# Optimization experiments

Hardware: AMD Instinct MI355X
Metric: run time of the kernel (lower is better)

The kernel has to match this reference:

```python
import jax, jax.numpy as jnp
import numpy as np

HIDDEN = 1024
N_HEADS = 16
N_LAYERS = 10
LOCAL_K = 3
TOKEN_T, TOKEN_H, TOKEN_W = 4, 16, 16
PATCH_SIZE = 2
LATENT_C = 16
TOKEN_DIM = LATENT_C * PATCH_SIZE * PATCH_SIZE  # 64
TOKEN_IN = TOKEN_DIM + 1                        # 65
N_TOKENS = TOKEN_T * TOKEN_H * TOKEN_W          # 1024
B = 1
HEAD_DIM = HIDDEN // N_HEADS
LN_EPS = 1e-5


def layer_norm(x, w, b):
    m = x.mean(-1, keepdims=True)
    v = ((x - m) ** 2).mean(-1, keepdims=True)
    return (x - m) * jax.lax.rsqrt(v + LN_EPS) * w + b


def patchify(lat):
    Bx, T, C, H, W = lat.shape
    ph, pw = H // PATCH_SIZE, W // PATCH_SIZE
    x = lat.reshape(Bx, T, C, ph, PATCH_SIZE, pw, PATCH_SIZE)
    x = x.transpose(0, 1, 3, 5, 2, 4, 6)
    return x.reshape(Bx, T * ph * pw, C * PATCH_SIZE * PATCH_SIZE)


def unpatchify(tok):
    Bx = tok.shape[0]
    C = TOKEN_DIM // (PATCH_SIZE * PATCH_SIZE)
    x = tok.reshape(Bx, TOKEN_T, TOKEN_H, TOKEN_W, C, PATCH_SIZE, PATCH_SIZE)
    x = x.transpose(0, 1, 4, 2, 5, 3, 6)
    return x.reshape(Bx, TOKEN_T, C, TOKEN_H * PATCH_SIZE, TOKEN_W * PATCH_SIZE)


def gather_neighbors(kv):
    # kv: (B, N, 2D) -> (B, N, 27, 2D), 3x3x3 zero-padded neighborhoods
    Bx, Nx, D2 = kv.shape
    pad = LOCAL_K // 2
    x = kv.reshape(Bx, TOKEN_T, TOKEN_H, TOKEN_W, D2)
    x = jnp.pad(x, ((0, 0), (pad, pad), (pad, pad), (pad, pad), (0, 0)))
    sl = [x[:, dt:dt + TOKEN_T, dh:dh + TOKEN_H, dw:dw + TOKEN_W]
          for dt in range(LOCAL_K) for dh in range(LOCAL_K) for dw in range(LOCAL_K)]
    nb = jnp.stack(sl, axis=4)  # (B,T,H,W,27,2D)
    return nb.reshape(Bx, Nx, LOCAL_K ** 3, D2)


def local_attention(x, qkv_w, out_w):
    Bx, Nx, D = x.shape
    H, d = N_HEADS, HEAD_DIM
    qkv = x @ qkv_w                       # (B,N,3D)
    q, k, v = jnp.split(qkv, 3, axis=-1)
    kv_nb = gather_neighbors(jnp.concatenate([k, v], axis=-1))  # (B,N,27,2D)
    k_nb, v_nb = jnp.split(kv_nb, 2, axis=-1)
    q = q.reshape(Bx, Nx, H, d)
    k_nb = k_nb.reshape(Bx, Nx, LOCAL_K ** 3, H, d)
    v_nb = v_nb.reshape(Bx, Nx, LOCAL_K ** 3, H, d)
    scores = jnp.einsum('bnhd,bnkhd->bnhk', q, k_nb) / np.sqrt(d).astype(np.float32)
    probs = jax.nn.softmax(scores, axis=-1)
    out = jnp.einsum('bnhk,bnkhd->bnhd', probs, v_nb).reshape(Bx, Nx, D)
    return out @ out_w


def global_attention(x, mask_flat, qkv_w, out_w):
    # Each masked query attends to all N keys; math identical to the
    # gather/SDPA/scatter in the original (per-query attention is independent),
    # realized as full attention masked to zero at unmasked positions.
    Bx, Nx, D = x.shape
    H, d = N_HEADS, HEAD_DIM
    qkv = x @ qkv_w
    q, k, v = jnp.split(qkv, 3, axis=-1)
    q = q.reshape(Bx, Nx, H, d)
    k = k.reshape(Bx, Nx, H, d)
    v = v.reshape(Bx, Nx, H, d)
    scores = jnp.einsum('bqhd,bkhd->bhqk', q, k) / np.sqrt(d).astype(np.float32)
    probs = jax.nn.softmax(scores, axis=-1)
    out = jnp.einsum('bhqk,bkhd->bqhd', probs, v).reshape(Bx, Nx, D)
    out = out @ out_w
    return out * mask_flat[..., None].astype(out.dtype)


def setup_inputs() -> dict:
    key = jax.random.key(0)
    ks = jax.random.split(key, 24)
    s = 0.02
    L, D = N_LAYERS, HIDDEN
    inp = {
        'latents': jax.random.normal(ks[0], (B, TOKEN_T, LATENT_C, TOKEN_H * PATCH_SIZE, TOKEN_W * PATCH_SIZE), jnp.float32),
        'token_mask': jax.random.uniform(ks[1], (B, TOKEN_T, TOKEN_H, TOKEN_W)) < 0.1,
        'input_proj_w': jax.random.normal(ks[2], (TOKEN_IN, D), jnp.float32) * s,
        'input_proj_b': jnp.zeros((D,), jnp.float32),
        'emb_t': jax.random.normal(ks[3], (TOKEN_T, D), jnp.float32) * s,
        'emb_h': jax.random.normal(ks[4], (TOKEN_H, D), jnp.float32) * s,
        'emb_w': jax.random.normal(ks[5], (TOKEN_W, D), jnp.float32) * s,
        'ln_local_w': jnp.ones((L, D), jnp.float32),
        'ln_local_b': jnp.zeros((L, D), jnp.float32),
        'ln_global_w': jnp.ones((L, D), jnp.float32),
        'ln_global_b': jnp.zeros((L, D), jnp.float32),
        'ln_ffn_w': jnp.ones((L, D), jnp.float32),
        'ln_ffn_b': jnp.zeros((L, D), jnp.float32),
        'local_qkv_w': jax.random.normal(ks[6], (L, D, 3 * D), jnp.float32) * s,
        'local_out_w': jax.random.normal(ks[7], (L, D, D), jnp.float32) * s,
        'global_qkv_w': jax.random.normal(ks[8], (L, D, 3 * D), jnp.float32) * s,
        'global_out_w': jax.random.normal(ks[9], (L, D, D), jnp.float32) * s,
        'ffn_w1': jax.random.normal(ks[10], (L, D, 4 * D), jnp.float32) * s,
        'ffn_b1': jnp.zeros((L, 4 * D), jnp.float32),
        'ffn_w2': jax.random.normal(ks[11], (L, 4 * D, D), jnp.float32) * s,
        'ffn_b2': jnp.zeros((L, D), jnp.float32),
        'final_ln_w': jnp.ones((D,), jnp.float32),
        'final_ln_b': jnp.zeros((D,), jnp.float32),
        # original zero-inits output_proj; use small random so the test is non-trivial
        'out_proj_w': jax.random.normal(ks[12], (D, TOKEN_DIM), jnp.float32) * s,
        'out_proj_b': jnp.zeros((TOKEN_DIM,), jnp.float32),
    }
    return inp


def reference(latents, token_mask, input_proj_w, input_proj_b, emb_t, emb_h, emb_w,
              ln_local_w, ln_local_b, ln_global_w, ln_global_b, ln_ffn_w, ln_ffn_b,
              local_qkv_w, local_out_w, global_qkv_w, global_out_w,
              ffn_w1, ffn_b1, ffn_w2, ffn_b2, final_ln_w, final_ln_b,
              out_proj_w, out_proj_b):
    Bx = latents.shape[0]
    mask_flat = token_mask.reshape(Bx, -1)
    tokens = patchify(latents)                       # (B, N, TOKEN_DIM)
    flag = mask_flat[..., None].astype(tokens.dtype)
    x = jnp.concatenate([tokens, flag], axis=-1) @ input_proj_w + input_proj_b

    tt, hh, ww = jnp.meshgrid(jnp.arange(TOKEN_T), jnp.arange(TOKEN_H), jnp.arange(TOKEN_W), indexing='ij')
    pos = emb_t[tt.reshape(-1)] + emb_h[hh.reshape(-1)] + emb_w[ww.reshape(-1)]
    x = x + pos[None]

    for l in range(N_LAYERS):
        x = x + local_attention(layer_norm(x, ln_local_w[l], ln_local_b[l]), local_qkv_w[l], local_out_w[l])
        x = x + global_attention(layer_norm(x, ln_global_w[l], ln_global_b[l]), mask_flat, global_qkv_w[l], global_out_w[l])
        h = layer_norm(x, ln_ffn_w[l], ln_ffn_b[l])
        h = jax.nn.gelu(h @ ffn_w1[l] + ffn_b1[l], approximate=False) @ ffn_w2[l] + ffn_b2[l]
        x = x + h

    delta = layer_norm(x, final_ln_w, final_ln_b) @ out_proj_w + out_proj_b
    return unpatchify(tokens + delta)
```

## Files before the change

kernel.cpp:

```cpp
#include <hip/hip_runtime.h>
#include <hip/hip_bf16.h>
#include <math.h>

typedef __bf16 bf16;
typedef __bf16 bf16x8 __attribute__((ext_vector_type(8)));
typedef __bf16 bf16x4 __attribute__((ext_vector_type(4)));
typedef float  f32x4 __attribute__((ext_vector_type(4)));
typedef unsigned int u32x4 __attribute__((ext_vector_type(4)));

#define NTOK 1024
#define HID  1024
#define NH   16
#define HD   64
#define NL   10
#define QCMAX 256

#define EPI_F32  0
#define EPI_GELU 1

__global__ __launch_bounds__(256)
void wtrans_k(const float* __restrict__ W, bf16* __restrict__ Wt, int K, int N)
{
    __shared__ bf16 tile[64][72];
    const long mofs = (long)blockIdx.z * K * N;
    const float* Ws = W + mofs;
    bf16* Wo = Wt + mofs;
    const int n0 = blockIdx.x * 64, k0 = blockIdx.y * 64;
    const int t = threadIdx.x;
    {
        const int r = t >> 2, cc = (t & 3) * 16;
        const float* src = Ws + (long)(k0 + r) * N + n0 + cc;
#pragma unroll
        for (int i = 0; i < 2; ++i) {
            f32x4 a = *(const f32x4*)(src + i * 8);
            f32x4 b = *(const f32x4*)(src + i * 8 + 4);
            bf16x8 w;
            w[0]=(bf16)a.x; w[1]=(bf16)a.y; w[2]=(bf16)a.z; w[3]=(bf16)a.w;
            w[4]=(bf16)b.x; w[5]=(bf16)b.y; w[6]=(bf16)b.z; w[7]=(bf16)b.w;
            *(bf16x8*)&tile[r][cc + i * 8] = w;
        }
    }
    __syncthreads();
    {
        const int n = t >> 2, kc = (t & 3) * 16;
        bf16x8 o0, o1;
#pragma unroll
        for (int j = 0; j < 8; ++j) { o0[j] = tile[kc + j][n]; o1[j] = tile[kc + 8 + j][n]; }
        bf16* dst = Wo + (long)(n0 + n) * K + k0 + kc;
        *(bf16x8*)dst = o0;
        *(bf16x8*)(dst + 8) = o1;
    }
}

template<int EPI, int BM, int BN, int KSPLIT>
__global__ __launch_bounds__(256)
void gemm_k(const bf16* __restrict__ A, int lda, long bsA,
            const bf16* __restrict__ Bt, int ldb, long bsB,
            void* __restrict__ Cv, int ldc, long bsC,
            const float* __restrict__ bias, int K)
{
    constexpr int WC  = (BM == 128) ? 2 : 4;
    constexpr int WTN = BN / WC;
    constexpr int NF  = WTN / 16;
    __shared__ bf16 Al[2][BM * 32];
    __shared__ bf16 Bl[2][BN * 32];

    const int t    = threadIdx.x;
    const int lane = t & 63;
    const int wv   = t >> 6;
    const int wr   = wv / WC, wc = wv % WC;
    const int lrow = lane & 15, lk = lane >> 4;
    const int n0   = blockIdx.x * BN;
    const int m0   = blockIdx.y * BM;
    const int ks   = (KSPLIT > 1) ? (blockIdx.z % KSPLIT) : 0;
    const int bz   = (KSPLIT > 1) ? (blockIdx.z / KSPLIT) : blockIdx.z;
    const int Kc   = K / KSPLIT;

    const bf16* Ab = A  + bsA * bz + (long)ks * Kc;
    const bf16* Bb = Bt + bsB * bz + (long)ks * Kc;

    f32x4 acc[4][NF];
#pragma unroll
    for (int m = 0; m < 4; ++m)
#pragma unroll
        for (int n = 0; n < NF; ++n) acc[m][n] = f32x4{0.f, 0.f, 0.f, 0.f};

    const int sr = t >> 2, sc = (t & 3) * 8;

    auto stage = [&](int buf, int kk) {
#pragma unroll
        for (int i = 0; i < BM / 64; ++i)
            __builtin_amdgcn_global_load_lds(
                (const __attribute__((address_space(1))) void*)(Ab + (long)(m0 + sr + i * 64) * lda + kk + sc),
                (__attribute__((address_space(3))) void*)(&Al[buf][i * 2048 + t * 8]), 16, 0, 0);
#pragma unroll
        for (int i = 0; i < BN / 64; ++i)
            __builtin_amdgcn_global_load_lds(
                (const __attribute__((address_space(1))) void*)(Bb + (long)(n0 + sr + i * 64) * ldb + kk + sc),
                (__attribute__((address_space(3))) void*)(&Bl[buf][i * 2048 + t * 8]), 16, 0, 0);
    };

    stage(0, 0);
    __syncthreads();
    int cur = 0;
    for (int k0 = 0; k0 < Kc; k0 += 32) {
        if (k0 + 32 < Kc) stage(cur ^ 1, k0 + 32);
        bf16x8 af[4], bfv[NF];
#pragma unroll
        for (int m = 0; m < 4; ++m)
            af[m] = *(const bf16x8*)&Al[cur][(wr * 64 + m * 16 + lrow) * 32 + lk * 8];
#pragma unroll
        for (int n = 0; n < NF; ++n)
            bfv[n] = *(const bf16x8*)&Bl[cur][(wc * WTN + n * 16 + lrow) * 32 + lk * 8];
#pragma unroll
        for (int m = 0; m < 4; ++m)
#pragma unroll
            for (int n = 0; n < NF; ++n)
                acc[m][n] = __builtin_amdgcn_mfma_f32_16x16x32_bf16(af[m], bfv[n], acc[m][n], 0, 0, 0);
        __syncthreads();
        cur ^= 1;
    }

    float* Cf = (float*)Cv + bsC * blockIdx.z;
    bf16*  Cb = (bf16*)Cv + bsC * blockIdx.z;
#pragma unroll
    for (int m = 0; m < 4; ++m)
#pragma unroll
        for (int n = 0; n < NF; ++n) {
            const int c = n0 + wc * WTN + n * 16 + lrow;
#pragma unroll
            for (int q = 0; q < 4; ++q) {
                const int r = m0 + wr * 64 + m * 16 + lk * 4 + q;
                const float v = acc[m][n][q];
                const long off = (long)r * ldc + c;
                if (EPI == EPI_F32) Cf[off] = v;
                else {
                    float u = v + bias[c];
                    Cb[off] = (bf16)(0.5f * u * (1.f + erff(u * 0.70710678118654752f)));
                }
            }
        }
}

template<int NS, bool BIAS, bool SCATTER>
__global__ __launch_bounds__(256)
void ln_add_k(float* __restrict__ x, const float* __restrict__ parts, long pstride,
              const float* __restrict__ bias, const int* __restrict__ rmap,
              const float* __restrict__ w, const float* __restrict__ b,
              bf16* __restrict__ o)
{
    int row  = blockIdx.x * 4 + (threadIdx.x >> 6);
    int lane = threadIdx.x & 63;
    f32x4* xr = (f32x4*)(x + (long)row * HID) + lane * 4;
    f32x4 v[4];
#pragma unroll
    for (int i = 0; i < 4; ++i) v[i] = xr[i];

    if (NS > 0) {
        int prow = SCATTER ? rmap[row] : row;
        if (!SCATTER || prow >= 0) {
            const float* pp = parts + (long)prow * 1024 + lane * 16;
#pragma unroll
            for (int ksi = 0; ksi < NS; ++ksi) {
                const f32x4* q = (const f32x4*)(pp + (long)ksi * pstride);
#pragma unroll
                for (int i = 0; i < 4; ++i) v[i] += q[i];
            }
            if (BIAS) {
                const f32x4* bb = (const f32x4*)bias + lane * 4;
#pragma unroll
                for (int i = 0; i < 4; ++i) v[i] += bb[i];
            }
#pragma unroll
            for (int i = 0; i < 4; ++i) xr[i] = v[i];
        }
    }

    float s = 0.f;
#pragma unroll
    for (int i = 0; i < 4; ++i) s += v[i].x + v[i].y + v[i].z + v[i].w;
    for (int m = 32; m; m >>= 1) s += __shfl_xor(s, m);
    float mean = s * (1.f / 1024.f);
    f32x4 d[4];
    float ss = 0.f;
#pragma unroll
    for (int i = 0; i < 4; ++i) {
        d[i] = v[i] - mean;
        ss += d[i].x * d[i].x + d[i].y * d[i].y + d[i].z * d[i].z + d[i].w * d[i].w;
    }
    for (int m = 32; m; m >>= 1) ss += __shfl_xor(ss, m);
    float rs = rsqrtf(ss * (1.f / 1024.f) + 1e-5f);
    const f32x4* wp = (const f32x4*)w + lane * 4;
    const f32x4* bp = (const f32x4*)b + lane * 4;
    bf16x8 o0, o1;
#pragma unroll
    for (int i = 0; i < 4; ++i) {
        f32x4 wv = wp[i], bv = bp[i];
        f32x4 e;
        e.x = d[i].x * rs * wv.x + bv.x; e.y = d[i].y * rs * wv.y + bv.y;
        e.z = d[i].z * rs * wv.z + bv.z; e.w = d[i].w * rs * wv.w + bv.w;
        if (i < 2) { o0[i*4+0]=(bf16)e.x; o0[i*4+1]=(bf16)e.y; o0[i*4+2]=(bf16)e.z; o0[i*4+3]=(bf16)e.w; }
        else       { int k=(i-2)*4; o1[k+0]=(bf16)e.x; o1[k+1]=(bf16)e.y; o1[k+2]=(bf16)e.z; o1[k+3]=(bf16)e.w; }
    }
    bf16* op = o + (long)row * HID + lane * 16;
    *(bf16x8*)op = o0;
    *(bf16x8*)(op + 8) = o1;
}

__global__ __launch_bounds__(256)
void red4pv_k(const float* __restrict__ p, bf16* __restrict__ Oc)
{
    int i = blockIdx.x * 256 + threadIdx.x;
    int d4 = (i & 15) * 4;
    int r  = (i >> 4) & 255;
    int h  = i >> 12;
    const float* base = p + (long)(h * 4) * 16384 + r * 64 + d4;
    f32x4 s = *(const f32x4*)base;
    s += *(const f32x4*)(base + 16384);
    s += *(const f32x4*)(base + 32768);
    s += *(const f32x4*)(base + 49152);
    bf16x4 o;
    o[0] = (bf16)s.x; o[1] = (bf16)s.y; o[2] = (bf16)s.z; o[3] = (bf16)s.w;
    *(bf16x4*)(Oc + (long)r * 1024 + h * 64 + d4) = o;
}

__global__ __launch_bounds__(256)
void lattn_k(const float* __restrict__ qkv, bf16* __restrict__ ao)
{
    int w    = blockIdx.x * 4 + (threadIdx.x >> 6);
    int lane = threadIdx.x & 63;
    int n = w >> 4, h = w & 15;
    int tt = n >> 8, hh = (n >> 4) & 15, ww = n & 15;

    int nj = -1;
    float dotv = 0.f;
    if (lane < 27) {
        int dt = lane / 9 - 1, dh = (lane % 9) / 3 - 1, dw = lane % 3 - 1;
        int t2 = tt + dt, h2 = hh + dh, w2 = ww + dw;
        if (t2 >= 0 && t2 < 4 && h2 >= 0 && h2 < 16 && w2 >= 0 && w2 < 16)
            nj = (t2 << 8) | (h2 << 4) | w2;
    }
    if (nj >= 0) {
        const f32x4* qp = (const f32x4*)(qkv + (long)n * 3072 + h * 64);
        const f32x4* kp = (const f32x4*)(qkv + (long)nj * 3072 + 1024 + h * 64);
#pragma unroll
        for (int i = 0; i < 16; ++i) {
            f32x4 q4 = qp[i], k4 = kp[i];
            dotv += q4.x * k4.x + q4.y * k4.y + q4.z * k4.z + q4.w * k4.w;
        }
    }
    float sc = (lane < 27) ? dotv * 0.125f : -3.0e38f;
    float mx = sc;
    for (int m = 32; m; m >>= 1) mx = fmaxf(mx, __shfl_xor(mx, m));
    float e = (lane < 27) ? __expf(sc - mx) : 0.f;
    float s = e;
    for (int m = 32; m; m >>= 1) s += __shfl_xor(s, m);
    float p = e / s;

    float acc = 0.f;
    for (int j = 0; j < 27; ++j) {
        float pj = __shfl(p, j);
        int  njj = __shfl(nj, j);
        if (njj >= 0) acc += pj * qkv[(long)njj * 3072 + 2048 + h * 64 + lane];
    }
    ao[(long)n * 1024 + h * 64 + lane] = (bf16)acc;
}

__global__ void compact_k(const int* __restrict__ mask, int* __restrict__ qidx,
                          int* __restrict__ rmap)
{
    int lane = threadIdx.x;
    int total = 0;
    for (int base = 0; base < 1024; base += 64) {
        int m = (mask[base + lane] != 0) ? 1 : 0;
        unsigned long long bal = __ballot(m);
        int pos = total + (int)__popcll(bal & ((1ull << lane) - 1ull));
        int ok = (m && pos < QCMAX);
        if (ok) qidx[pos] = base + lane;
        rmap[base + lane] = ok ? pos : -1;
        total += (int)__popcll(bal);
    }
    for (int i = total + lane; i < QCMAX; i += 64) qidx[i] = -1;
}

__global__ __launch_bounds__(256)
void qkvbuild_k(const float* __restrict__ qkv, const int* __restrict__ qidx,
                bf16* __restrict__ Qc, bf16* __restrict__ Kh, bf16* __restrict__ Vt)
{
    __shared__ bf16 vt[64][72];
    const int h = blockIdx.y;
    const int t = threadIdx.x;
    if (blockIdx.x < 4) {
        const int r = blockIdx.x * 64 + (t >> 2), dc = (t & 3) * 16;
        const int q = qidx[r];
        bf16x8 o0, o1;
        if (q >= 0) {
            const f32x4* src = (const f32x4*)(qkv + (long)q * 3072 + h * 64 + dc);
#pragma unroll
            for (int i = 0; i < 2; ++i) {
                f32x4 a = src[i * 2] * 0.125f, b = src[i * 2 + 1] * 0.125f;
                bf16x8 w;
                w[0]=(bf16)a.x; w[1]=(bf16)a.y; w[2]=(bf16)a.z; w[3]=(bf16)a.w;
                w[4]=(bf16)b.x; w[5]=(bf16)b.y; w[6]=(bf16)b.z; w[7]=(bf16)b.w;
                if (i == 0) o0 = w; else o1 = w;
            }
        } else {
#pragma unroll
            for (int j = 0; j < 8; ++j) { o0[j] = (bf16)0.f; o1[j] = (bf16)0.f; }
        }
        bf16* dst = Qc + (long)h * (QCMAX * 64) + (long)r * 64 + dc;
        *(bf16x8*)dst = o0;
        *(bf16x8*)(dst + 8) = o1;
        return;
    }
    const int k0 = (blockIdx.x - 4) * 64;
    {
        const int r = t >> 2, dc = (t & 3) * 16;
        const float* kp = qkv + (long)(k0 + r) * 3072 + 1024 + h * 64 + dc;
        const float* vp = kp + 1024;
        bf16x8 ko0, ko1;
#pragma unroll
        for (int i = 0; i < 2; ++i) {
            f32x4 a = *(const f32x4*)(kp + i * 8);
            f32x4 b = *(const f32x4*)(kp + i * 8 + 4);
            bf16x8 w;
            w[0]=(bf16)a.x; w[1]=(bf16)a.y; w[2]=(bf16)a.z; w[3]=(bf16)a.w;
            w[4]=(bf16)b.x; w[5]=(bf16)b.y; w[6]=(bf16)b.z; w[7]=(bf16)b.w;
            if (i == 0) ko0 = w; else ko1 = w;
        }
        bf16* kd = Kh + (long)h * (NTOK * 64) + (long)(k0 + r) * 64 + dc;
        *(bf16x8*)kd = ko0;
        *(bf16x8*)(kd + 8) = ko1;
#pragma unroll
        for (int i = 0; i < 2; ++i) {
            f32x4 a = *(const f32x4*)(vp + i * 8);
            f32x4 b = *(const f32x4*)(vp + i * 8 + 4);
            bf16x8 w;
            w[0]=(bf16)a.x; w[1]=(bf16)a.y; w[2]=(bf16)a.z; w[3]=(bf16)a.w;
            w[4]=(bf16)b.x; w[5]=(bf16)b.y; w[6]=(bf16)b.z; w[7]=(bf16)b.w;
            *(bf16x8*)&vt[r][dc + i * 8] = w;
        }
    }
    __syncthreads();
    {
        const int d = t >> 2, kc = (t & 3) * 16;
        bf16x8 o0, o1;
#pragma unroll
        for (int j = 0; j < 8; ++j) { o0[j] = vt[kc + j][d]; o1[j] = vt[kc + 8 + j][d]; }
        bf16* dst = Vt + (long)h * (64 * NTOK) + (long)d * NTOK + k0 + kc;
        *(bf16x8*)dst = o0;
        *(bf16x8*)(dst + 8) = o1;
    }
}

__global__ __launch_bounds__(256)
void softmax_k(const float* __restrict__ S, bf16* __restrict__ P)
{
    int row  = blockIdx.x * 4 + (threadIdx.x >> 6);
    int lane = threadIdx.x & 63;
    const f32x4* sp = (const f32x4*)(S + (long)row * 1024) + lane * 4;
    f32x4 v[4];
#pragma unroll
    for (int i = 0; i < 4; ++i) v[i] = sp[i];
    float mx = -3.0e38f;
#pragma unroll
    for (int i = 0; i < 4; ++i)
        mx = fmaxf(mx, fmaxf(fmaxf(v[i].x, v[i].y), fmaxf(v[i].z, v[i].w)));
    for (int m = 32; m; m >>= 1) mx = fmaxf(mx, __shfl_xor(mx, m));
    f32x4 ev[4];
    float sum = 0.f;
#pragma unroll
    for (int i = 0; i < 4; ++i) {
        ev[i].x = __expf(v[i].x - mx); ev[i].y = __expf(v[i].y - mx);
        ev[i].z = __expf(v[i].z - mx); ev[i].w = __expf(v[i].w - mx);
        sum += ev[i].x + ev[i].y + ev[i].z + ev[i].w;
    }
    for (int m = 32; m; m >>= 1) sum += __shfl_xor(sum, m);
    float inv = 1.f / sum;
    bf16x8 o0, o1;
#pragma unroll
    for (int i = 0; i < 4; ++i) {
        f32x4 e = ev[i] * inv;
        if (i < 2) { o0[i*4+0]=(bf16)e.x; o0[i*4+1]=(bf16)e.y; o0[i*4+2]=(bf16)e.z; o0[i*4+3]=(bf16)e.w; }
        else       { int k=(i-2)*4; o1[k+0]=(bf16)e.x; o1[k+1]=(bf16)e.y; o1[k+2]=(bf16)e.z; o1[k+3]=(bf16)e.w; }
    }
    bf16* op = P + (long)row * 1024 + lane * 16;
    *(bf16x8*)op = o0;
    *(bf16x8*)(op + 8) = o1;
}

__global__ __launch_bounds__(256)
void prep_k(const float* __restrict__ lat, const int* __restrict__ mask,
            const float* __restrict__ Wi, const float* __restrict__ bi,
            const float* __restrict__ et, const float* __restrict__ eh,
            const float* __restrict__ ew,
            float* __restrict__ x, float* __restrict__ tokens)
{
    __shared__ float tl[16][65];
    int t = threadIdx.x;
    int n0 = blockIdx.x * 16;
    for (int idx = t; idx < 16 * 65; idx += 256) {
        int ti = idx / 65, d = idx % 65;
        int n = n0 + ti;
        int tt = n >> 8, hh = (n >> 4) & 15, wwi = n & 15;
        float v;
        if (d < 64) {
            int c = d >> 2, ph = (d >> 1) & 1, pw = d & 1;
            v = lat[(((long)tt * 16 + c) * 32 + hh * 2 + ph) * 32 + wwi * 2 + pw];
            tokens[(long)n * 64 + d] = v;
        } else {
            v = mask[n] ? 1.f : 0.f;
        }
        tl[ti][d] = v;
    }
    __syncthreads();
    f32x4 acc[16];
#pragma unroll
    for (int i = 0; i < 16; ++i) acc[i] = f32x4{0.f, 0.f, 0.f, 0.f};
    for (int d = 0; d < 65; ++d) {
        f32x4 wv = *(const f32x4*)(Wi + (long)d * 1024 + t * 4);
#pragma unroll
        for (int ti = 0; ti < 16; ++ti) acc[ti] += tl[ti][d] * wv;
    }
    f32x4 bb = *(const f32x4*)(bi + t * 4);
    for (int ti = 0; ti < 16; ++ti) {
        int n = n0 + ti;
        int tt = n >> 8, hh = (n >> 4) & 15, wwi = n & 15;
        f32x4 pos = *(const f32x4*)(et + (long)tt * 1024 + t * 4)
                  + *(const f32x4*)(eh + (long)hh * 1024 + t * 4)
                  + *(const f32x4*)(ew + (long)wwi * 1024 + t * 4);
        *(f32x4*)(x + (long)n * 1024 + t * 4) = acc[ti] + bb + pos;
    }
}

__global__ __launch_bounds__(256)
void final_k(const bf16* __restrict__ xn, const float* __restrict__ OW,
             const float* __restrict__ ob, const float* __restrict__ tokens,
             float* __restrict__ out)
{
    __shared__ bf16 xl[8][1024];
    __shared__ float part[4][8][64];
    int t = threadIdx.x;
    int n0 = blockIdx.x * 8;
    for (int i = t; i < 1024; i += 256)
        ((u32x4*)xl)[i] = ((const u32x4*)(xn + (long)n0 * 1024))[i];
    __syncthreads();
    int j = t & 63, s = t >> 6;
    float acc[8] = {0.f, 0.f, 0.f, 0.f, 0.f, 0.f, 0.f, 0.f};
    for (int k = s * 256; k < s * 256 + 256; ++k) {
        float w = OW[(long)k * 64 + j];
#pragma unroll
        for (int ti = 0; ti < 8; ++ti) acc[ti] += (float)xl[ti][k] * w;
    }
    for (int ti = 0; ti < 8; ++ti) part[s][ti][j] = acc[ti];
    __syncthreads();
    if (s == 0) {
        for (int ti = 0; ti < 8; ++ti) {
            int n = n0 + ti;
            float v = part[0][ti][j] + part[1][ti][j] + part[2][ti][j] + part[3][ti][j]
                    + ob[j] + tokens[(long)n * 64 + j];
            int tt = n >> 8, hh = (n >> 4) & 15, wwi = n & 15;
            int c = j >> 2, ph = (j >> 1) & 1, pw = j & 1;
            out[(((long)tt * 16 + c) * 32 + hh * 2 + ph) * 32 + wwi * 2 + pw] = v;
        }
    }
}

extern "C" void kernel_launch(void* const* d_in, const int* in_sizes, int n_in,
                              void* d_out, int out_size, void* d_ws, size_t ws_size,
                              hipStream_t stream)
{
    const float* latents = (const float*)d_in[0];
    const int*   mask    = (const int*)d_in[1];
    const float* ipw  = (const float*)d_in[2];
    const float* ipb  = (const float*)d_in[3];
    const float* et   = (const float*)d_in[4];
    const float* eh   = (const float*)d_in[5];
    const float* ew   = (const float*)d_in[6];
    const float* lnlw = (const float*)d_in[7];
    const float* lnlb = (const float*)d_in[8];
    const float* lngw = (const float*)d_in[9];
    const float* lngb = (const float*)d_in[10];
    const float* lnfw = (const float*)d_in[11];
    const float* lnfb = (const float*)d_in[12];
    const float* lqkv = (const float*)d_in[13];
    const float* lout = (const float*)d_in[14];
    const float* gqkv = (const float*)d_in[15];
    const float* gout = (const float*)d_in[16];
    const float* w1   = (const float*)d_in[17];
    const float* b1   = (const float*)d_in[18];
    const float* w2   = (const float*)d_in[19];
    const float* b2   = (const float*)d_in[20];
    const float* flw  = (const float*)d_in[21];
    const float* flb  = (const float*)d_in[22];
    const float* opw  = (const float*)d_in[23];
    const float* opb  = (const float*)d_in[24];

    char* p = (char*)d_ws;
    auto alloc = [&](size_t bytes) { char* r = p; p += (bytes + 255) & ~(size_t)255; return r; };
    float* x      = (float*)alloc((size_t)4 << 20);
    bf16*  xn     = (bf16*)alloc((size_t)2 << 20);
    float* qkv    = (float*)alloc((size_t)12 << 20);
    bf16*  ao     = (bf16*)alloc((size_t)2 << 20);
    bf16*  hbuf   = (bf16*)alloc((size_t)8 << 20);
    float* tokens = (float*)alloc((size_t)256 << 10);
    bf16*  Qc     = (bf16*)alloc((size_t)512 << 10);
    bf16*  Kh     = (bf16*)alloc((size_t)2 << 20);
    bf16*  Vt     = (bf16*)alloc((size_t)2 << 20);
    float* S      = (float*)alloc((size_t)16 << 20);
    bf16*  P      = (bf16*)alloc((size_t)8 << 20);
    bf16*  Oc     = (bf16*)alloc((size_t)512 << 10);
    int*   qidx   = (int*)alloc(4096);
    int*   rmap   = (int*)alloc(4096);
    float* loutp = (float*)alloc((size_t)2 * 1024 * 1024 * 4);
    float* goutp = (float*)alloc((size_t)8 * 256 * 1024 * 4);
    float* pvp   = (float*)alloc((size_t)64 * 256 * 64 * 4);
    float* f2p   = (float*)alloc((size_t)4 * 1024 * 1024 * 4);
    bf16* lqkvT = (bf16*)alloc((size_t)10 * 3072 * 1024 * 2);
    bf16* loutT = (bf16*)alloc((size_t)10 * 1024 * 1024 * 2);
    bf16* gqkvT = (bf16*)alloc((size_t)10 * 3072 * 1024 * 2);
    bf16* goutT = (bf16*)alloc((size_t)10 * 1024 * 1024 * 2);
    bf16* w1T   = (bf16*)alloc((size_t)10 * 4096 * 1024 * 2);
    bf16* w2T   = (bf16*)alloc((size_t)10 * 1024 * 4096 * 2);

    wtrans_k<<<dim3(48, 16, NL), 256, 0, stream>>>(lqkv, lqkvT, 1024, 3072);
    wtrans_k<<<dim3(16, 16, NL), 256, 0, stream>>>(lout, loutT, 1024, 1024);
    wtrans_k<<<dim3(48, 16, NL), 256, 0, stream>>>(gqkv, gqkvT, 1024, 3072);
    wtrans_k<<<dim3(16, 16, NL), 256, 0, stream>>>(gout, goutT, 1024, 1024);
    wtrans_k<<<dim3(64, 16, NL), 256, 0, stream>>>(w1, w1T, 1024, 4096);
    wtrans_k<<<dim3(16, 64, NL), 256, 0, stream>>>(w2, w2T, 4096, 1024);

    prep_k<<<64, 256, 0, stream>>>(latents, mask, ipw, ipb, et, eh, ew, x, tokens);
    compact_k<<<1, 64, 0, stream>>>(mask, qidx, rmap);

    for (int l = 0; l < NL; ++l) {
        const long wq  = (long)l * 3072 * 1024;
        const long wo  = (long)l * 1024 * 1024;
        const long wf1 = (long)l * 4096 * 1024;

        if (l == 0)
            ln_add_k<0, false, false><<<256, 256, 0, stream>>>(
                x, nullptr, 0, nullptr, nullptr, lnlw, lnlb, xn);
        else
            ln_add_k<4, true, false><<<256, 256, 0, stream>>>(
                x, f2p, (long)1024 * 1024, b2 + (l - 1) * 1024, nullptr,
                lnlw + l * HID, lnlb + l * HID, xn);

        gemm_k<EPI_F32, 64, 128, 1><<<dim3(24, 16, 1), 256, 0, stream>>>(
            xn, 1024, 0, lqkvT + wq, 1024, 0, qkv, 3072, 0, nullptr, 1024);
        lattn_k<<<4096, 256, 0, stream>>>(qkv, ao);
        gemm_k<EPI_F32, 64, 128, 2><<<dim3(8, 16, 2), 256, 0, stream>>>(
            ao, 1024, 0, loutT + wo, 1024, 0, loutp, 1024, (long)1024 * 1024, nullptr, 1024);

        ln_add_k<2, false, false><<<256, 256, 0, stream>>>(
            x, loutp, (long)1024 * 1024, nullptr, nullptr,
            lngw + l * HID, lngb + l * HID, xn);

        gemm_k<EPI_F32, 64, 128, 1><<<dim3(24, 16, 1), 256, 0, stream>>>(
            xn, 1024, 0, gqkvT + wq, 1024, 0, qkv, 3072, 0, nullptr, 1024);
        qkvbuild_k<<<dim3(20, 16), 256, 0, stream>>>(qkv, qidx, Qc, Kh, Vt);
        gemm_k<EPI_F32, 64, 128, 1><<<dim3(8, 4, 16), 256, 0, stream>>>(
            Qc, 64, (long)256 * 64, Kh, 64, (long)1024 * 64,
            S, 1024, (long)256 * 1024, nullptr, 64);
        softmax_k<<<1024, 256, 0, stream>>>(S, P);
        gemm_k<EPI_F32, 64, 64, 4><<<dim3(1, 4, 64), 256, 0, stream>>>(
            P, 1024, (long)256 * 1024, Vt, 1024, (long)64 * 1024,
            pvp, 64, (long)256 * 64, nullptr, 1024);
        red4pv_k<<<256, 256, 0, stream>>>(pvp, Oc);
        gemm_k<EPI_F32, 64, 128, 8><<<dim3(8, 4, 8), 256, 0, stream>>>(
            Oc, 1024, 0, goutT + wo, 1024, 0, goutp, 1024, (long)256 * 1024, nullptr, 1024);

        ln_add_k<8, false, true><<<256, 256, 0, stream>>>(
            x, goutp, (long)256 * 1024, nullptr, rmap,
            lnfw + l * HID, lnfb + l * HID, xn);

        gemm_k<EPI_GELU, 64, 128, 1><<<dim3(32, 16, 1), 256, 0, stream>>>(
            xn, 1024, 0, w1T + wf1, 1024, 0, hbuf, 4096, 0, b1 + l * 4096, 1024);
        gemm_k<EPI_F32, 64, 128, 4><<<dim3(8, 16, 4), 256, 0, stream>>>(
            hbuf, 4096, 0, w2T + wf1, 4096, 0, f2p, 1024, (long)1024 * 1024, nullptr, 4096);
    }

    ln_add_k<4, true, false><<<256, 256, 0, stream>>>(
        x, f2p, (long)1024 * 1024, b2 + 9 * 1024, nullptr, flw, flb, xn);
    final_k<<<128, 256, 0, stream>>>(xn, opw, opb, tokens, (float*)d_out);
}
```

Baseline: 2.225 ms.

## Store QKV in bf16, fuse local out-proj residual, merge weight transposes

Both QKV GEMMs now write bf16 output instead of fp32, which halves QKV traffic for the local attention and qkvbuild kernels. The local output projection drops its split-K and adds straight into x through a residual epilogue, removing the partial buffer and the reduction in the next layernorm. The six weight-transpose launches become one kernel with an XOR-swizzled shared tile to cut bank conflicts. In exchange, q and k are rounded to bf16 before the local attention dot products, and the out-proj GEMM launches fewer blocks.

```diff
diff --git a/kernel.cpp b/kernel.cpp
--- a/kernel.cpp
+++ b/kernel.cpp
@@ -10,42 +10,65 @@
 
 #define NTOK 1024
 #define HID  1024
-#define NH   16
-#define HD   64
 #define NL   10
 #define QCMAX 256
 
-#define EPI_F32  0
-#define EPI_GELU 1
-
-__global__ __launch_bounds__(256)
-void wtrans_k(const float* __restrict__ W, bf16* __restrict__ Wt, int K, int N)
-{
-    __shared__ bf16 tile[64][72];
+#define EPI_F32   0
+#define EPI_GELU  1
+#define EPI_RESID 2
+#define EPI_BF16  3
+
+__global__ __launch_bounds__(256)
+void wtransall_k(const float* __restrict__ lqkv, const float* __restrict__ lout,
+                 const float* __restrict__ gqkv, const float* __restrict__ gout,
+                 const float* __restrict__ w1,   const float* __restrict__ w2,
+                 bf16* __restrict__ lqkvT, bf16* __restrict__ loutT,
+                 bf16* __restrict__ gqkvT, bf16* __restrict__ goutT,
+                 bf16* __restrict__ w1T,   bf16* __restrict__ w2T)
+{
+    __shared__ bf16 tile[64 * 64];
+    const int b = blockIdx.x;
+    const float* W; bf16* O; int K, N, ti;
+    if      (b < 768)  { W = lqkv; O = lqkvT; K = 1024; N = 3072; ti = b; }
+    else if (b < 1024) { W = lout; O = loutT; K = 1024; N = 1024; ti = b - 768; }
+    else if (b < 1792) { W = gqkv; O = gqkvT; K = 1024; N = 3072; ti = b - 1024; }
+    else if (b < 2048) { W = gout; O = goutT; K = 1024; N = 1024; ti = b - 1792; }
+    else if (b < 3072) { W = w1;   O = w1T;   K = 1024; N = 4096; ti = b - 2048; }
+    else               { W = w2;   O = w2T;   K = 4096; N = 1024; ti = b - 3072; }
+    const int ntx = N >> 6;
+    const int n0 = (ti % ntx) * 64, k0 = (ti / ntx) * 64;
     const long mofs = (long)blockIdx.z * K * N;
     const float* Ws = W + mofs;
-    bf16* Wo = Wt + mofs;
-    const int n0 = blockIdx.x * 64, k0 = blockIdx.y * 64;
+    bf16* Wo = O + mofs;
     const int t = threadIdx.x;
     {
         const int r = t >> 2, cc = (t & 3) * 16;
+        const int x = (r >> 3) & 7;
+        const int g0 = cc >> 3;
         const float* src = Ws + (long)(k0 + r) * N + n0 + cc;
-#pragma unroll
-        for (int i = 0; i < 2; ++i) {
-            f32x4 a = *(const f32x4*)(src + i * 8);
-            f32x4 b = *(const f32x4*)(src + i * 8 + 4);
-            bf16x8 w;
-            w[0]=(bf16)a.x; w[1]=(bf16)a.y; w[2]=(bf16)a.z; w[3]=(bf16)a.w;
-            w[4]=(bf16)b.x; w[5]=(bf16)b.y; w[6]=(bf16)b.z; w[7]=(bf16)b.w;
-            *(bf16x8*)&tile[r][cc + i * 8] = w;
-        }
+        f32x4 a0 = *(const f32x4*)(src);
+        f32x4 a1 = *(const f32x4*)(src + 4);
+        f32x4 a2 = *(const f32x4*)(src + 8);
+        f32x4 a3 = *(const f32x4*)(src + 12);
+        bf16x8 w0, w1v;
+        w0[0]=(bf16)a0.x; w0[1]=(bf16)a0.y; w0[2]=(bf16)a0.z; w0[3]=(bf16)a0.w;
+        w0[4]=(bf16)a1.x; w0[5]=(bf16)a1.y; w0[6]=(bf16)a1.z; w0[7]=(bf16)a1.w;
+        w1v[0]=(bf16)a2.x; w1v[1]=(bf16)a2.y; w1v[2]=(bf16)a2.z; w1v[3]=(bf16)a2.w;
+        w1v[4]=(bf16)a3.x; w1v[5]=(bf16)a3.y; w1v[6]=(bf16)a3.z; w1v[7]=(bf16)a3.w;
+        *(bf16x8*)&tile[r * 64 + ((g0    ) ^ x) * 8] = w0;
+        *(bf16x8*)&tile[r * 64 + ((g0 | 1) ^ x) * 8] = w1v;
     }
     __syncthreads();
     {
         const int n = t >> 2, kc = (t & 3) * 16;
+        const int g = n >> 3, no = n & 7;
         bf16x8 o0, o1;
 #pragma unroll
-        for (int j = 0; j < 8; ++j) { o0[j] = tile[kc + j][n]; o1[j] = tile[kc + 8 + j][n]; }
+        for (int j = 0; j < 8; ++j) {
+            int r0 = kc + j, r1 = kc + 8 + j;
+            o0[j] = tile[r0 * 64 + ((g ^ ((r0 >> 3) & 7)) * 8) + no];
+            o1[j] = tile[r1 * 64 + ((g ^ ((r1 >> 3) & 7)) * 8) + no];
+        }
         bf16* dst = Wo + (long)(n0 + n) * K + k0 + kc;
         *(bf16x8*)dst = o0;
         *(bf16x8*)(dst + 8) = o1;
@@ -133,7 +156,9 @@
                 const int r = m0 + wr * 64 + m * 16 + lk * 4 + q;
                 const float v = acc[m][n][q];
                 const long off = (long)r * ldc + c;
-                if (EPI == EPI_F32) Cf[off] = v;
+                if (EPI == EPI_F32)        Cf[off] = v;
+                else if (EPI == EPI_BF16)  Cb[off] = (bf16)v;
+                else if (EPI == EPI_RESID) Cf[off] += v;
                 else {
                     float u = v + bias[c];
                     Cb[off] = (bf16)(0.5f * u * (1.f + erff(u * 0.70710678118654752f)));
@@ -225,7 +250,7 @@
 }
 
 __global__ __launch_bounds__(256)
-void lattn_k(const float* __restrict__ qkv, bf16* __restrict__ ao)
+void lattn_k(const bf16* __restrict__ qkv, bf16* __restrict__ ao)
 {
     int w    = blockIdx.x * 4 + (threadIdx.x >> 6);
     int lane = threadIdx.x & 63;
@@ -241,12 +266,13 @@
             nj = (t2 << 8) | (h2 << 4) | w2;
     }
     if (nj >= 0) {
-        const f32x4* qp = (const f32x4*)(qkv + (long)n * 3072 + h * 64);
-        const f32x4* kp = (const f32x4*)(qkv + (long)nj * 3072 + 1024 + h * 64);
-#pragma unroll
-        for (int i = 0; i < 16; ++i) {
-            f32x4 q4 = qp[i], k4 = kp[i];
-            dotv += q4.x * k4.x + q4.y * k4.y + q4.z * k4.z + q4.w * k4.w;
+        const bf16x8* qp = (const bf16x8*)(qkv + (long)n * 3072 + h * 64);
+        const bf16x8* kp = (const bf16x8*)(qkv + (long)nj * 3072 + 1024 + h * 64);
+#pragma unroll
+        for (int i = 0; i < 8; ++i) {
+            bf16x8 q8 = qp[i], k8 = kp[i];
+#pragma unroll
+            for (int j = 0; j < 8; ++j) dotv += (float)q8[j] * (float)k8[j];
         }
     }
     float sc = (lane < 27) ? dotv * 0.125f : -3.0e38f;
@@ -261,7 +287,7 @@
     for (int j = 0; j < 27; ++j) {
         float pj = __shfl(p, j);
         int  njj = __shfl(nj, j);
-        if (njj >= 0) acc += pj * qkv[(long)njj * 3072 + 2048 + h * 64 + lane];
+        if (njj >= 0) acc += pj * (float)qkv[(long)njj * 3072 + 2048 + h * 64 + lane];
     }
     ao[(long)n * 1024 + h * 64 + lane] = (bf16)acc;
 }
@@ -284,7 +310,7 @@
 }
 
 __global__ __launch_bounds__(256)
-void qkvbuild_k(const float* __restrict__ qkv, const int* __restrict__ qidx,
+void qkvbuild_k(const bf16* __restrict__ qkv, const int* __restrict__ qidx,
                 bf16* __restrict__ Qc, bf16* __restrict__ Kh, bf16* __restrict__ Vt)
 {
     __shared__ bf16 vt[64][72];
@@ -295,14 +321,12 @@
         const int q = qidx[r];
         bf16x8 o0, o1;
         if (q >= 0) {
-            const f32x4* src = (const f32x4*)(qkv + (long)q * 3072 + h * 64 + dc);
-#pragma unroll
-            for (int i = 0; i < 2; ++i) {
-                f32x4 a = src[i * 2] * 0.125f, b = src[i * 2 + 1] * 0.125f;
-                bf16x8 w;
-                w[0]=(bf16)a.x; w[1]=(bf16)a.y; w[2]=(bf16)a.z; w[3]=(bf16)a.w;
-                w[4]=(bf16)b.x; w[5]=(bf16)b.y; w[6]=(bf16)b.z; w[7]=(bf16)b.w;
-                if (i == 0) o0 = w; else o1 = w;
+            const bf16x8* src = (const bf16x8*)(qkv + (long)q * 3072 + h * 64 + dc);
+            bf16x8 a = src[0], b = src[1];
+#pragma unroll
+            for (int j = 0; j < 8; ++j) {
+                o0[j] = (bf16)((float)a[j] * 0.125f);
+                o1[j] = (bf16)((float)b[j] * 0.125f);
             }
         } else {
 #pragma unroll
@@ -316,30 +340,14 @@
     const int k0 = (blockIdx.x - 4) * 64;
     {
         const int r = t >> 2, dc = (t & 3) * 16;
-        const float* kp = qkv + (long)(k0 + r) * 3072 + 1024 + h * 64 + dc;
-        const float* vp = kp + 1024;
-        bf16x8 ko0, ko1;
-#pragma unroll
-        for (int i = 0; i < 2; ++i) {
-            f32x4 a = *(const f32x4*)(kp + i * 8);
-            f32x4 b = *(const f32x4*)(kp + i * 8 + 4);
-            bf16x8 w;
-            w[0]=(bf16)a.x; w[1]=(bf16)a.y; w[2]=(bf16)a.z; w[3]=(bf16)a.w;
-            w[4]=(bf16)b.x; w[5]=(bf16)b.y; w[6]=(bf16)b.z; w[7]=(bf16)b.w;
-            if (i == 0) ko0 = w; else ko1 = w;
-        }
+        const bf16x8* kp = (const bf16x8*)(qkv + (long)(k0 + r) * 3072 + 1024 + h * 64 + dc);
+        const bf16x8* vp = (const bf16x8*)(qkv + (long)(k0 + r) * 3072 + 2048 + h * 64 + dc);
+        bf16x8 k0v = kp[0], k1v = kp[1];
         bf16* kd = Kh + (long)h * (NTOK * 64) + (long)(k0 + r) * 64 + dc;
-        *(bf16x8*)kd = ko0;
-        *(bf16x8*)(kd + 8) = ko1;
-#pragma unroll
-        for (int i = 0; i < 2; ++i) {
-            f32x4 a = *(const f32x4*)(vp + i * 8);
-            f32x4 b = *(const f32x4*)(vp + i * 8 + 4);
-            bf16x8 w;
-            w[0]=(bf16)a.x; w[1]=(bf16)a.y; w[2]=(bf16)a.z; w[3]=(bf16)a.w;
-            w[4]=(bf16)b.x; w[5]=(bf16)b.y; w[6]=(bf16)b.z; w[7]=(bf16)b.w;
-            *(bf16x8*)&vt[r][dc + i * 8] = w;
-        }
+        *(bf16x8*)kd = k0v;
+        *(bf16x8*)(kd + 8) = k1v;
+        *(bf16x8*)&vt[r][dc]     = vp[0];
+        *(bf16x8*)&vt[r][dc + 8] = vp[1];
     }
     __syncthreads();
     {
@@ -500,7 +508,7 @@
     auto alloc = [&](size_t bytes) { char* r = p; p += (bytes + 255) & ~(size_t)255; return r; };
     float* x      = (float*)alloc((size_t)4 << 20);
     bf16*  xn     = (bf16*)alloc((size_t)2 << 20);
-    float* qkv    = (float*)alloc((size_t)12 << 20);
+    bf16*  qkvb   = (bf16*)alloc((size_t)6 << 20);
     bf16*  ao     = (bf16*)alloc((size_t)2 << 20);
     bf16*  hbuf   = (bf16*)alloc((size_t)8 << 20);
     float* tokens = (float*)alloc((size_t)256 << 10);
@@ -512,10 +520,9 @@
     bf16*  Oc     = (bf16*)alloc((size_t)512 << 10);
     int*   qidx   = (int*)alloc(4096);
     int*   rmap   = (int*)alloc(4096);
-    float* loutp = (float*)alloc((size_t)2 * 1024 * 1024 * 4);
-    float* goutp = (float*)alloc((size_t)8 * 256 * 1024 * 4);
-    float* pvp   = (float*)alloc((size_t)64 * 256 * 64 * 4);
-    float* f2p   = (float*)alloc((size_t)4 * 1024 * 1024 * 4);
+    float* goutp  = (float*)alloc((size_t)8 * 256 * 1024 * 4);
+    float* pvp    = (float*)alloc((size_t)64 * 256 * 64 * 4);
+    float* f2p    = (float*)alloc((size_t)4 * 1024 * 1024 * 4);
     bf16* lqkvT = (bf16*)alloc((size_t)10 * 3072 * 1024 * 2);
     bf16* loutT = (bf16*)alloc((size_t)10 * 1024 * 1024 * 2);
     bf16* gqkvT = (bf16*)alloc((size_t)10 * 3072 * 1024 * 2);
@@ -523,12 +530,8 @@
     bf16* w1T   = (bf16*)alloc((size_t)10 * 4096 * 1024 * 2);
     bf16* w2T   = (bf16*)alloc((size_t)10 * 1024 * 4096 * 2);
 
-    wtrans_k<<<dim3(48, 16, NL), 256, 0, stream>>>(lqkv, lqkvT, 1024, 3072);
-    wtrans_k<<<dim3(16, 16, NL), 256, 0, stream>>>(lout, loutT, 1024, 1024);
-    wtrans_k<<<dim3(48, 16, NL), 256, 0, stream>>>(gqkv, gqkvT, 1024, 3072);
-    wtrans_k<<<dim3(16, 16, NL), 256, 0, stream>>>(gout, goutT, 1024, 1024);
-    wtrans_k<<<dim3(64, 16, NL), 256, 0, stream>>>(w1, w1T, 1024, 4096);
-    wtrans_k<<<dim3(16, 64, NL), 256, 0, stream>>>(w2, w2T, 4096, 1024);
+    wtransall_k<<<dim3(4096, 1, NL), 256, 0, stream>>>(
+        lqkv, lout, gqkv, gout, w1, w2, lqkvT, loutT, gqkvT, goutT, w1T, w2T);
 
     prep_k<<<64, 256, 0, stream>>>(latents, mask, ipw, ipb, et, eh, ew, x, tokens);
     compact_k<<<1, 64, 0, stream>>>(mask, qidx, rmap);
@@ -546,19 +549,18 @@
                 x, f2p, (long)1024 * 1024, b2 + (l - 1) * 1024, nullptr,
                 lnlw + l * HID, lnlb + l * HID, xn);
 
-        gemm_k<EPI_F32, 64, 128, 1><<<dim3(24, 16, 1), 256, 0, stream>>>(
-            xn, 1024, 0, lqkvT + wq, 1024, 0, qkv, 3072, 0, nullptr, 1024);
-        lattn_k<<<4096, 256, 0, stream>>>(qkv, ao);
-        gemm_k<EPI_F32, 64, 128, 2><<<dim3(8, 16, 2), 256, 0, stream>>>(
-            ao, 1024, 0, loutT + wo, 1024, 0, loutp, 1024, (long)1024 * 1024, nullptr, 1024);
-
-        ln_add_k<2, false, false><<<256, 256, 0, stream>>>(
-            x, loutp, (long)1024 * 1024, nullptr, nullptr,
-            lngw + l * HID, lngb + l * HID, xn);
-
-        gemm_k<EPI_F32, 64, 128, 1><<<dim3(24, 16, 1), 256, 0, stream>>>(
-            xn, 1024, 0, gqkvT + wq, 1024, 0, qkv, 3072, 0, nullptr, 1024);
-        qkvbuild_k<<<dim3(20, 16), 256, 0, stream>>>(qkv, qidx, Qc, Kh, Vt);
+        gemm_k<EPI_BF16, 64, 128, 1><<<dim3(24, 16, 1), 256, 0, stream>>>(
+            xn, 1024, 0, lqkvT + wq, 1024, 0, qkvb, 3072, 0, nullptr, 1024);
+        lattn_k<<<4096, 256, 0, stream>>>(qkvb, ao);
+        gemm_k<EPI_RESID, 64, 128, 1><<<dim3(8, 16, 1), 256, 0, stream>>>(
+            ao, 1024, 0, loutT + wo, 1024, 0, x, 1024, 0, nullptr, 1024);
+
+        ln_add_k<0, false, false><<<256, 256, 0, stream>>>(
+            x, nullptr, 0, nullptr, nullptr, lngw + l * HID, lngb + l * HID, xn);
+
+        gemm_k<EPI_BF16, 64, 128, 1><<<dim3(24, 16, 1), 256, 0, stream>>>(
+            xn, 1024, 0, gqkvT + wq, 1024, 0, qkvb, 3072, 0, nullptr, 1024);
+        qkvbuild_k<<<dim3(20, 16), 256, 0, stream>>>(qkvb, qidx, Qc, Kh, Vt);
         gemm_k<EPI_F32, 64, 128, 1><<<dim3(8, 4, 16), 256, 0, stream>>>(
             Qc, 64, (long)256 * 64, Kh, 64, (long)1024 * 64,
             S, 1024, (long)256 * 1024, nullptr, 64);
```

New measurement: 2.232 ms. About the same (+0.3%).
